# Kernel optimization log

Measured on AMD Instinct MI355X. Metric: run time of the kernel, lower is better.

The kernel has to match this reference:

```python
import jax, jax.numpy as jnp
import numpy as np

B = 16; L_IN = 512; D_MODEL = 512; N_HEAD = 8; D_K = 128; D_V = 128
D_FF = 2048; N_LAYER = 4; WINDOW = (4, 4, 4); INNER = 5; COV = 4; NUM_SEQ = 128
N_LVL = len(WINDOW) + 1


def _build_mask_sizes():
    # Pyraformer get_mask: intra-scale band + inter-scale parent/child links.
    all_size = [L_IN]
    for w in WINDOW:
        all_size.append(all_size[-1] // w)
    L = sum(all_size)
    vis = np.zeros((L, L), dtype=bool)
    iw = INNER // 2
    starts = [0]
    for s in all_size:
        starts.append(starts[-1] + s)
    for li, sz in enumerate(all_size):
        s = starts[li]
        for i in range(s, s + sz):
            vis[i, max(i - iw, s):min(i + iw + 1, s + sz)] = True
    for li in range(1, len(all_size)):
        s = starts[li]
        for i in range(s, s + all_size[li]):
            l = (s - all_size[li - 1]) + (i - s) * WINDOW[li - 1]
            if i == s + all_size[li] - 1:
                r = s
            else:
                r = (s - all_size[li - 1]) + (i - s + 1) * WINDOW[li - 1]
            vis[i, l:r] = True
            vis[l:r, i] = True
    return ~vis, all_size  # True = blocked


def _build_indexes(all_size):
    # Pyraformer refer_points: for each fine position, its ancestor at each scale.
    idx = np.zeros((L_IN, len(all_size)), dtype=np.int64)
    for i in range(L_IN):
        idx[i, 0] = i
        former = i
        for j in range(1, len(all_size)):
            start = sum(all_size[:j])
            inner = former - (start - all_size[j - 1])
            former = start + min(inner // WINDOW[j - 1], all_size[j] - 1)
            idx[i, j] = former
    return idx


def _layer_norm(x, g, b, eps=1e-5):
    m = x.mean(-1, keepdims=True)
    v = x.var(-1, keepdims=True)
    return (x - m) / jnp.sqrt(v + eps) * g + b


def _conv1d(x, w, stride):  # x: [B,C,L], w: [O,I,K]
    return jax.lax.conv_general_dilated(x, w, (stride,), 'VALID',
                                        dimension_numbers=('NCH', 'OIH', 'NCH'))


def _forward(x, cov_w, cov_b, data_conv_w, down_w, down_b, conv_w, conv_b, bn_g, bn_b,
             up_w, up_b, bln_g, bln_b, wq, wk, wv, fc_w, ln1_g, ln1_b,
             ffn_w1, ffn_b1, ffn_w2, ffn_b2, ln2_g, ln2_b, attn_mask, gather_idx):
    Bsz = x.shape[0]
    # SingleStepEmbedding
    covs = jnp.concatenate([x[:, :, 1:1 + COV], (x[:, :, -1] / NUM_SEQ - 0.5)[..., None]], -1)
    cov_emb = covs @ cov_w + cov_b
    data = x[:, :, 0][:, None, :]                      # [B,1,L]
    data = jnp.concatenate([data[:, :, -1:], data, data[:, :, :1]], -1)  # circular pad k=3
    data_emb = _conv1d(data, data_conv_w, 1).transpose(0, 2, 1)          # [B,L,D]
    i = jnp.arange(D_MODEL)
    vec = jnp.power(10000.0, 2.0 * (i // 2) / D_MODEL)
    ang = jnp.arange(L_IN)[:, None] / vec
    pos_emb = jnp.where(i % 2 == 0, jnp.sin(ang), jnp.cos(ang))
    seq = cov_emb + data_emb + pos_emb[None]
    # Bottleneck_Construct (down -> strided convs -> up -> concat -> LN)
    tmp = (seq @ down_w + down_b).transpose(0, 2, 1)   # [B,d_k,L]
    outs = []
    for s in range(len(WINDOW)):
        tmp = _conv1d(tmp, conv_w[s], WINDOW[s]) + conv_b[s][None, :, None]
        mu = tmp.mean((0, 2), keepdims=True)
        var = tmp.var((0, 2), keepdims=True)
        tmp = (tmp - mu) / jnp.sqrt(var + 1e-5) * bn_g[s][None, :, None] + bn_b[s][None, :, None]
        tmp = jax.nn.elu(tmp)
        outs.append(tmp)
    pyr = jnp.concatenate(outs, axis=2).transpose(0, 2, 1) @ up_w + up_b
    enc = _layer_norm(jnp.concatenate([seq, pyr], axis=1), bln_g, bln_b)  # [B,Ltot,D]
    Lt = enc.shape[1]
    scale = np.float32(1.0 / np.sqrt(D_K))
    for l in range(N_LAYER):
        q = (enc @ wq[l]).reshape(Bsz, Lt, N_HEAD, D_K).transpose(0, 2, 1, 3)
        k = (enc @ wk[l]).reshape(Bsz, Lt, N_HEAD, D_K).transpose(0, 2, 1, 3)
        v = (enc @ wv[l]).reshape(Bsz, Lt, N_HEAD, D_V).transpose(0, 2, 1, 3)
        scores = jnp.einsum('bhqd,bhkd->bhqk', q, k) * scale
        scores = jnp.where(attn_mask[None, None], -1e9, scores)
        attn = jax.nn.softmax(scores, -1)
        o = jnp.einsum('bhqk,bhkd->bhqd', attn, v).transpose(0, 2, 1, 3).reshape(Bsz, Lt, N_HEAD * D_V)
        enc = _layer_norm(o @ fc_w[l] + enc, ln1_g[l], ln1_b[l])  # post-norm
        h = jax.nn.gelu(enc @ ffn_w1[l] + ffn_b1[l], approximate=False) @ ffn_w2[l] + ffn_b2[l]
        enc = _layer_norm(enc + h, ln2_g[l], ln2_b[l])
    # refer_points gather: [B, L_IN, N_LVL*D]
    out = enc[:, gather_idx.reshape(-1), :].reshape(Bsz, L_IN, N_LVL * D_MODEL)
    return out


def setup_inputs() -> dict:
    key = jax.random.key(0)
    ks = iter(jax.random.split(key, 64))

    def nrm(shape, scale=0.02):
        return (jax.random.normal(next(ks), shape) * scale).astype(jnp.float32)

    covs = jax.random.normal(next(ks), (B, L_IN, COV + 1), jnp.float32)
    ids = jax.random.randint(next(ks), (B, L_IN), 0, NUM_SEQ).astype(jnp.float32)
    x = jnp.concatenate([covs, ids[..., None]], -1)  # col0=data, 1..COV=covs, last=series id
    mask_np, all_size = _build_mask_sizes()
    idx = _build_indexes(all_size)
    nw = len(WINDOW)
    return dict(
        x=x,
        cov_w=nrm((COV + 1, D_MODEL)), cov_b=jnp.zeros((D_MODEL,), jnp.float32),
        data_conv_w=nrm((D_MODEL, 1, 3)),
        down_w=nrm((D_MODEL, D_K)), down_b=jnp.zeros((D_K,), jnp.float32),
        conv_w=nrm((nw, D_K, D_K, WINDOW[0])), conv_b=jnp.zeros((nw, D_K), jnp.float32),
        bn_g=jnp.ones((nw, D_K), jnp.float32), bn_b=jnp.zeros((nw, D_K), jnp.float32),
        up_w=nrm((D_K, D_MODEL)), up_b=jnp.zeros((D_MODEL,), jnp.float32),
        bln_g=jnp.ones((D_MODEL,), jnp.float32), bln_b=jnp.zeros((D_MODEL,), jnp.float32),
        wq=nrm((N_LAYER, D_MODEL, N_HEAD * D_K)), wk=nrm((N_LAYER, D_MODEL, N_HEAD * D_K)),
        wv=nrm((N_LAYER, D_MODEL, N_HEAD * D_V)), fc_w=nrm((N_LAYER, N_HEAD * D_V, D_MODEL)),
        ln1_g=jnp.ones((N_LAYER, D_MODEL), jnp.float32), ln1_b=jnp.zeros((N_LAYER, D_MODEL), jnp.float32),
        ffn_w1=nrm((N_LAYER, D_MODEL, D_FF)), ffn_b1=jnp.zeros((N_LAYER, D_FF), jnp.float32),
        ffn_w2=nrm((N_LAYER, D_FF, D_MODEL)), ffn_b2=jnp.zeros((N_LAYER, D_MODEL), jnp.float32),
        ln2_g=jnp.ones((N_LAYER, D_MODEL), jnp.float32), ln2_b=jnp.zeros((N_LAYER, D_MODEL), jnp.float32),
        attn_mask=jnp.asarray(mask_np),
        gather_idx=jnp.asarray(idx),
    )


def reference(x, cov_w, cov_b, data_conv_w, down_w, down_b, conv_w, conv_b, bn_g, bn_b,
              up_w, up_b, bln_g, bln_b, wq, wk, wv, fc_w, ln1_g, ln1_b,
              ffn_w1, ffn_b1, ffn_w2, ffn_b2, ln2_g, ln2_b, attn_mask, gather_idx):
    return _forward(x, cov_w, cov_b, data_conv_w, down_w, down_b, conv_w, conv_b, bn_g, bn_b,
                    up_w, up_b, bln_g, bln_b, wq, wk, wv, fc_w, ln1_g, ln1_b,
                    ffn_w1, ffn_b1, ffn_w2, ffn_b2, ln2_g, ln2_b, attn_mask, gather_idx)
```

## Files before the change

kernel.cpp:

```cpp
#include <hip/hip_runtime.h>
#include <math.h>

typedef unsigned short u16;
typedef unsigned int u32;
typedef __attribute__((ext_vector_type(8))) short s16x8;
typedef __attribute__((ext_vector_type(4))) float f32x4;
typedef __attribute__((ext_vector_type(4))) u32 u32x4;
typedef __attribute__((ext_vector_type(2))) u32 u32x2;

#define LT 680

static __device__ __forceinline__ float bf2f(u16 u) {
  u32 v = ((u32)u) << 16;
  return __builtin_bit_cast(float, v);
}
static __device__ __forceinline__ u16 f2bf(float f) {
  u32 u = __builtin_bit_cast(u32, f);
  u32 r = (u + 0x7FFFu + ((u >> 16) & 1u)) >> 16;
  return (u16)r;
}
static __device__ __forceinline__ float lo16(u32 u) {
  return __builtin_bit_cast(float, u << 16);
}
static __device__ __forceinline__ float hi16(u32 u) {
  return __builtin_bit_cast(float, u & 0xFFFF0000u);
}

static __device__ __forceinline__ void gload16(const u16* g, u16* l) {
  __builtin_amdgcn_global_load_lds(
      (const __attribute__((address_space(1))) u32*)g,
      (__attribute__((address_space(3))) u32*)l, 16, 0, 0);
}

__global__ void detect_k(const u32* __restrict__ blng, int* __restrict__ flag) {
  if (threadIdx.x == 0 && blockIdx.x == 0)
    *flag = (blng[0] == 0x3F803F80u) ? 1 : 0;
}

struct CvtArgs {
  const void* src[20];
  float* dst[20];
  int pre[21];
};

__global__ __launch_bounds__(256) void cvtall_k(CvtArgs a, const int* __restrict__ flag) {
  int i = blockIdx.x * 256 + threadIdx.x;
  if (i >= a.pre[20]) return;
  int s = 0;
#pragma unroll
  for (int k = 1; k <= 20; ++k)
    if (i >= a.pre[k]) s = k;
  int j = i - a.pre[s];
  bool isb = (*flag != 0);
  a.dst[s][j] = isb ? bf2f(((const u16*)a.src[s])[j]) : ((const float*)a.src[s])[j];
}

__global__ __launch_bounds__(256) void tc2_k(const void* __restrict__ S,
                                             u16* __restrict__ D, int K, int N,
                                             size_t sstride, size_t dstride,
                                             const int* __restrict__ flag) {
  __shared__ u16 t[32][33];
  size_t soff = (size_t)blockIdx.z * sstride;
  D += (size_t)blockIdx.z * dstride;
  int nb = blockIdx.x * 32, kb = blockIdx.y * 32;
  int lx = threadIdx.x & 31, ly = threadIdx.x >> 5;
  bool isb = (*flag != 0);
#pragma unroll
  for (int i = 0; i < 4; ++i) {
    size_t idx = soff + (size_t)(kb + ly + 8 * i) * N + nb + lx;
    t[ly + 8 * i][lx] = isb ? ((const u16*)S)[idx] : f2bf(((const float*)S)[idx]);
  }
  __syncthreads();
#pragma unroll
  for (int i = 0; i < 4; ++i)
    D[(size_t)(nb + ly + 8 * i) * K + kb + lx] = t[lx][ly + 8 * i];
}

static __device__ __forceinline__ void reduce2_256(float& a, float& b, float* sm) {
#pragma unroll
  for (int o = 32; o; o >>= 1) { a += __shfl_xor(a, o); b += __shfl_xor(b, o); }
  int w = threadIdx.x >> 6, ln = threadIdx.x & 63;
  if (ln == 0) { sm[w] = a; sm[4 + w] = b; }
  __syncthreads();
  a = sm[0] + sm[1] + sm[2] + sm[3];
  b = sm[4] + sm[5] + sm[6] + sm[7];
  __syncthreads();
}

__global__ __launch_bounds__(256) void emb_k(
    const float* __restrict__ x, const float* __restrict__ covw,
    const float* __restrict__ covb, const float* __restrict__ dw,
    float* __restrict__ seq) {
  int r = blockIdx.x;
  int b = r >> 9, l = r & 511;
  int base = r * 6;
  float c0 = x[base + 1], c1 = x[base + 2];
  float c2 = x[base + 3], c3 = x[base + 4];
  float c4 = x[base + 5] * 0.0078125f - 0.5f;
  int lm = (l + 511) & 511, lp = (l + 1) & 511;
  float dm = x[((b << 9) + lm) * 6];
  float d0 = x[base];
  float dp = x[((b << 9) + lp) * 6];
  for (int d = threadIdx.x; d < 512; d += 256) {
    float cov = c0 * covw[d] + c1 * covw[512 + d] +
                c2 * covw[1024 + d] + c3 * covw[1536 + d] +
                c4 * covw[2048 + d] + covb[d];
    float cv = dm * dw[d * 3] + d0 * dw[d * 3 + 1] + dp * dw[d * 3 + 2];
    float ex = (float)(2 * (d >> 1)) * (1.0f / 512.0f);
    float vec = powf(10000.0f, ex);
    float ang = (float)l / vec;
    float pos = (d & 1) ? cosf(ang) : sinf(ang);
    seq[((size_t)r << 9) + d] = cov + cv + pos;
  }
}

__global__ void tconv_k(const float* __restrict__ w, float* __restrict__ wt) {
  int e = blockIdx.x * 256 + threadIdx.x;
  if (e >= 3 * 512 * 128) return;
  int o = e & 127, ik = (e >> 7) & 511, s = e >> 16;
  wt[e] = w[s * 65536 + o * 512 + ik];
}

__global__ __launch_bounds__(256) void gemm_k(
    const float* __restrict__ A, const float* __restrict__ Bw,
    const float* __restrict__ bias, float* __restrict__ C,
    int M, int N, int K, int act) {
  __shared__ float As[16][64];
  __shared__ float Bs[16][64];
  int tid = threadIdx.x;
  int m0 = blockIdx.y * 64, n0 = blockIdx.x * 64;
  int tx = tid & 15, ty = tid >> 4;
  int la_r = tid >> 2, la_c = (tid & 3) << 2;
  int lb_r = tid >> 4, lb_c = (tid & 15) << 2;
  float acc[4][4] = {};
  for (int k0 = 0; k0 < K; k0 += 16) {
    float4 av = *reinterpret_cast<const float4*>(A + (size_t)(m0 + la_r) * K + k0 + la_c);
    As[la_c + 0][la_r] = av.x;
    As[la_c + 1][la_r] = av.y;
    As[la_c + 2][la_r] = av.z;
    As[la_c + 3][la_r] = av.w;
    float4 bv = *reinterpret_cast<const float4*>(Bw + (size_t)(k0 + lb_r) * N + n0 + lb_c);
    Bs[lb_r][lb_c + 0] = bv.x;
    Bs[lb_r][lb_c + 1] = bv.y;
    Bs[lb_r][lb_c + 2] = bv.z;
    Bs[lb_r][lb_c + 3] = bv.w;
    __syncthreads();
#pragma unroll
    for (int kk = 0; kk < 16; ++kk) {
      float4 a4 = *reinterpret_cast<const float4*>(&As[kk][ty << 2]);
      float4 b4 = *reinterpret_cast<const float4*>(&Bs[kk][tx << 2]);
      float ar[4] = {a4.x, a4.y, a4.z, a4.w};
      float br[4] = {b4.x, b4.y, b4.z, b4.w};
#pragma unroll
      for (int i = 0; i < 4; ++i)
#pragma unroll
        for (int j = 0; j < 4; ++j) acc[i][j] = fmaf(ar[i], br[j], acc[i][j]);
    }
    __syncthreads();
  }
  float bj[4] = {0.f, 0.f, 0.f, 0.f};
  if (bias) {
#pragma unroll
    for (int j = 0; j < 4; ++j) bj[j] = bias[n0 + (tx << 2) + j];
  }
#pragma unroll
  for (int i = 0; i < 4; ++i) {
    float4 o;
    float* op = reinterpret_cast<float*>(&o);
#pragma unroll
    for (int j = 0; j < 4; ++j) op[j] = acc[i][j] + bj[j];
    *reinterpret_cast<float4*>(C + (size_t)(m0 + (ty << 2) + i) * N + n0 + (tx << 2)) = o;
  }
}

static __device__ __forceinline__ f32x4 mfma16(s16x8 a, s16x8 b, f32x4 c) {
  return __builtin_amdgcn_mfma_f32_16x16x32_bf16(a, b, c, 0, 0, 0);
}

__global__ __launch_bounds__(256) void mgemm_k(
    const u16* __restrict__ A, const u16* __restrict__ BT,
    const float* __restrict__ bias, void* __restrict__ C,
    int M, int N, int K, int flags) {
  __shared__ char smem[32768];
  float* st = (float*)smem;
  int tid = threadIdx.x;

  int nN = N >> 7;
  int nwg = gridDim.x;
  int bid = blockIdx.x;
  int qq = nwg >> 3, rr = nwg & 7;
  int xcd = bid & 7, lin = bid >> 3;
  int s_ = (xcd < rr ? xcd * (qq + 1) : rr * (qq + 1) + (xcd - rr) * qq) + lin;
  int m0 = (s_ / nN) << 7, n0 = (s_ % nN) << 7;

  int l = tid & 63, wid = tid >> 6;
  int wr = wid >> 1, wc = wid & 1;
  f32x4 acc[4][4];
#pragma unroll
  for (int i = 0; i < 4; ++i)
#pragma unroll
    for (int j = 0; j < 4; ++j)
#pragma unroll
      for (int r = 0; r < 4; ++r) acc[i][j][r] = 0.f;

  int L8 = l >> 3;
  int p0_ = (l & 7) ^ L8;
  int rloc = 2 * L8 + (p0_ >> 2);
  int cel = (p0_ & 3) << 3;
  const u16* Ag0 = A + (size_t)m0 * K;
  const u16* Bg0 = BT + (size_t)n0 * K;

  auto STAGE = [&](int c, int kt) {
    u16* Ad = (u16*)smem + c * 8192;
    u16* Bd = Ad + 4096;
#pragma unroll
    for (int i = 0; i < 2; ++i) {
      int rg = wid * 32 + i * 16 + rloc;
      gload16(Ag0 + (size_t)rg * K + kt + cel, &Ad[(wid * 16 + i * 8) * 64]);
      gload16(Bg0 + (size_t)rg * K + kt + cel, &Bd[(wid * 16 + i * 8) * 64]);
    }
  };

  int sfrag = (((l & 1) << 2) + (l >> 4)) ^ (((l & 15) >> 1));
  int lhalf = (l & 15) >> 1;

  int nt = K >> 5;
  STAGE(0, 0);
  for (int t = 0; t < nt; ++t) {
    int cur = t & 1;
    if (t + 1 < nt) {
      STAGE(cur ^ 1, (t + 1) << 5);
      asm volatile("s_waitcnt vmcnt(4)" ::: "memory");
    } else {
      asm volatile("s_waitcnt vmcnt(0)" ::: "memory");
    }
    __builtin_amdgcn_s_barrier();
    const u16* Asb = (const u16*)smem + cur * 8192;
    const u16* Bsb = Asb + 4096;
    s16x8 af[4];
#pragma unroll
    for (int fr = 0; fr < 4; ++fr)
      af[fr] = *reinterpret_cast<const s16x8*>(
          &Asb[(wr * 32 + fr * 8 + lhalf) * 64 + sfrag * 8]);
#pragma unroll
    for (int fc = 0; fc < 4; ++fc) {
      s16x8 bf = *reinterpret_cast<const s16x8*>(
          &Bsb[(wc * 32 + fc * 8 + lhalf) * 64 + sfrag * 8]);
#pragma unroll
      for (int fr = 0; fr < 4; ++fr)
        acc[fr][fc] = mfma16(af[fr], bf, acc[fr][fc]);
    }
    asm volatile("s_waitcnt lgkmcnt(0)" ::: "memory");
    __builtin_amdgcn_s_barrier();
  }

  int cl = l & 15, rg2 = l >> 4;
  float bj[4];
#pragma unroll
  for (int fc = 0; fc < 4; ++fc)
    bj[fc] = bias ? bias[n0 + wc * 64 + fc * 16 + cl] : 0.f;
  int sr2 = tid >> 3;
  int scg = (tid & 7) << 4;
  int growb = m0 + ((sr2 >> 4) << 6) + (sr2 & 15);
#pragma unroll
  for (int fr = 0; fr < 4; ++fr) {
#pragma unroll
    for (int fc = 0; fc < 4; ++fc) {
      int col = wc * 64 + fc * 16 + cl;
#pragma unroll
      for (int r = 0; r < 4; ++r) {
        float v = acc[fr][fc][r] + bj[fc];
        if (flags & 2) {
          float zz = 1.5957691f * fmaf(0.044715f * v, v * v, v);
          v = v / (1.0f + __expf(-zz));
        }
        st[(wr * 16 + rg2 * 4 + r) * 132 + col] = v;
      }
    }
    __syncthreads();
    int gr = growb + fr * 16;
    if (flags & 1) {
      u32x4 o0, o1;
      u16* p0 = (u16*)&o0; u16* p1 = (u16*)&o1;
#pragma unroll
      for (int i = 0; i < 8; ++i) p0[i] = f2bf(st[sr2 * 132 + scg + i]);
#pragma unroll
      for (int i = 0; i < 8; ++i) p1[i] = f2bf(st[sr2 * 132 + scg + 8 + i]);
      u16* dst = (u16*)C + (size_t)gr * N + n0 + scg;
      __builtin_nontemporal_store(o0, reinterpret_cast<u32x4*>(dst));
      __builtin_nontemporal_store(o1, reinterpret_cast<u32x4*>(dst + 8));
    } else {
      float* dst = (float*)C + (size_t)gr * N + n0 + scg;
#pragma unroll
      for (int i = 0; i < 4; ++i)
        __builtin_nontemporal_store(
            *reinterpret_cast<const f32x4*>(&st[sr2 * 132 + scg + 4 * i]),
            reinterpret_cast<f32x4*>(dst + 4 * i));
    }
    __syncthreads();
  }
}

__global__ __launch_bounds__(256) void mgemm64_k(
    const u16* __restrict__ A, const u16* __restrict__ BT,
    const float* __restrict__ bias, float* __restrict__ C,
    int M, int N, int K) {
  __shared__ char smem[49152];
  float* st = (float*)smem;
  int tid = threadIdx.x;

  int nN = N >> 6;
  int nwg = gridDim.x;
  int bid = blockIdx.x;
  int qq = nwg >> 3, rr = nwg & 7;
  int xcd = bid & 7, lin = bid >> 3;
  int s_ = (xcd < rr ? xcd * (qq + 1) : rr * (qq + 1) + (xcd - rr) * qq) + lin;
  int m0 = (s_ / nN) << 7, n0 = (s_ % nN) << 6;

  int l = tid & 63, wid = tid >> 6;
  f32x4 acc[2][4];
#pragma unroll
  for (int i = 0; i < 2; ++i)
#pragma unroll
    for (int j = 0; j < 4; ++j)
#pragma unroll
      for (int r = 0; r < 4; ++r) acc[i][j][r] = 0.f;

  int row8 = l >> 3, cp = l & 7;
  int cg = (cp ^ (row8 & 7)) << 3;
  const u16* Ag0 = A + (size_t)m0 * K;
  const u16* Bg0 = BT + (size_t)n0 * K;

  auto STAGE = [&](int c, int kt) {
    u16* Ad = (u16*)smem + c * 12288;
    u16* Bd = Ad + 8192;
    int rbA = wid * 32;
#pragma unroll
    for (int i = 0; i < 4; ++i) {
      int r = rbA + i * 8 + row8;
      gload16(Ag0 + (size_t)r * K + kt + cg, &Ad[(rbA + i * 8) * 64]);
    }
    int rbB = wid * 16;
#pragma unroll
    for (int i = 0; i < 2; ++i) {
      int r = rbB + i * 8 + row8;
      gload16(Bg0 + (size_t)r * K + kt + cg, &Bd[(rbB + i * 8) * 64]);
    }
  };

  int nt = K >> 6;
  STAGE(0, 0);
  for (int t = 0; t < nt; ++t) {
    int cur = t & 1;
    if (t + 1 < nt) {
      STAGE(cur ^ 1, (t + 1) << 6);
      asm volatile("s_waitcnt vmcnt(6)" ::: "memory");
    } else {
      asm volatile("s_waitcnt vmcnt(0)" ::: "memory");
    }
    __builtin_amdgcn_s_barrier();
    const u16* Asb = (const u16*)smem + cur * 12288;
    const u16* Bsb = Asb + 8192;
#pragma unroll
    for (int kk = 0; kk < 2; ++kk) {
      int kc = ((kk * 4 + (l >> 4)) ^ (l & 7)) * 8;
      s16x8 af[2];
#pragma unroll
      for (int fr = 0; fr < 2; ++fr)
        af[fr] = *reinterpret_cast<const s16x8*>(
            &Asb[(wid * 32 + fr * 16 + (l & 15)) * 64 + kc]);
#pragma unroll
      for (int fc = 0; fc < 4; ++fc) {
        s16x8 bf = *reinterpret_cast<const s16x8*>(
            &Bsb[(fc * 16 + (l & 15)) * 64 + kc]);
#pragma unroll
        for (int fr = 0; fr < 2; ++fr)
          acc[fr][fc] = mfma16(af[fr], bf, acc[fr][fc]);
      }
    }
    asm volatile("s_waitcnt lgkmcnt(0)" ::: "memory");
    __builtin_amdgcn_s_barrier();
  }

  int cl = l & 15, rg = l >> 4;
  float bj[4];
#pragma unroll
  for (int fc = 0; fc < 4; ++fc)
    bj[fc] = bias ? bias[n0 + fc * 16 + cl] : 0.f;
  int lr = tid >> 2;
  int lc = (tid & 3) << 4;
  int gr = m0 + ((lr >> 4) << 5) + (lr & 15);
#pragma unroll
  for (int fr = 0; fr < 2; ++fr) {
#pragma unroll
    for (int fc = 0; fc < 4; ++fc)
#pragma unroll
      for (int r = 0; r < 4; ++r)
        st[(wid * 16 + rg * 4 + r) * 68 + fc * 16 + cl] = acc[fr][fc][r] + bj[fc];
    __syncthreads();
    float* dst = C + (size_t)(gr + fr * 16) * N + n0 + lc;
#pragma unroll
    for (int i = 0; i < 4; ++i)
      __builtin_nontemporal_store(
          *reinterpret_cast<const f32x4*>(&st[lr * 68 + lc + 4 * i]),
          reinterpret_cast<f32x4*>(dst + 4 * i));
    __syncthreads();
  }
}

__global__ void im2col_k(const float* __restrict__ Y, float* __restrict__ X,
                         int Ti, int To) {
  int e = blockIdx.x * 256 + threadIdx.x;
  int ik = e & 511;
  int bt = e >> 9;
  int b = bt / To, t = bt - b * To;
  int i = ik >> 2, k = ik & 3;
  X[e] = Y[((size_t)(b * Ti + (t << 2) + k) << 7) + i];
}

__global__ __launch_bounds__(256) void bnelu_k(float* __restrict__ Y,
                                               const float* __restrict__ g,
                                               const float* __restrict__ be, int Ms) {
  __shared__ float sm[8];
  int ch = blockIdx.x;
  float s = 0.f, s2 = 0.f;
  for (int i = threadIdx.x; i < Ms; i += 256) {
    float v = Y[((size_t)i << 7) + ch];
    s += v; s2 += v * v;
  }
  reduce2_256(s, s2, sm);
  float mu = s / (float)Ms;
  float var = s2 / (float)Ms - mu * mu;
  float inv = rsqrtf(var + 1e-5f);
  float ga = g[ch], bb = be[ch];
  for (int i = threadIdx.x; i < Ms; i += 256) {
    float v = (Y[((size_t)i << 7) + ch] - mu) * inv * ga + bb;
    Y[((size_t)i << 7) + ch] = (v > 0.f) ? v : (expf(v) - 1.0f);
  }
}

__global__ void scat_k(const float* __restrict__ Y, float* __restrict__ cat,
                       int Ts, int off) {
  int e = blockIdx.x * 256 + threadIdx.x;
  int i = e & 127;
  int bt = e >> 7;
  int b = bt / Ts, t = bt - b * Ts;
  cat[((size_t)(b * 168 + off + t) << 7) + i] = Y[e];
}

__global__ __launch_bounds__(256) void catln_k(
    const float* __restrict__ seq, const float* __restrict__ pyr,
    const float* __restrict__ g, const float* __restrict__ be,
    float* __restrict__ out, u16* __restrict__ outb) {
  __shared__ float sm[8];
  int row = blockIdx.x;
  int b = row / LT, j = row - b * LT;
  const float* src = (j < 512) ? (seq + ((size_t)(b * 512 + j) << 9))
                               : (pyr + ((size_t)(b * 168 + j - 512) << 9));
  int t = threadIdx.x;
  float x0 = src[t], x1 = src[t + 256];
  float s = x0 + x1, s2 = x0 * x0 + x1 * x1;
  reduce2_256(s, s2, sm);
  float mu = s * 0.001953125f;
  float var = s2 * 0.001953125f - mu * mu;
  float inv = rsqrtf(var + 1e-5f);
  size_t ob = (size_t)row << 9;
  float v0 = (x0 - mu) * inv * g[t] + be[t];
  float v1 = (x1 - mu) * inv * g[t + 256] + be[t + 256];
  out[ob + t] = v0; out[ob + t + 256] = v1;
  outb[ob + t] = f2bf(v0); outb[ob + t + 256] = f2bf(v1);
}

__global__ __launch_bounds__(256) void lnres_k(
    const float* __restrict__ A, const float* __restrict__ R,
    const float* __restrict__ g, const float* __restrict__ be,
    float* __restrict__ O, u16* __restrict__ Ob) {
  __shared__ float sm[8];
  int row = blockIdx.x;
  size_t base = (size_t)row << 9;
  int t = threadIdx.x;
  float x0 = A[base + t] + R[base + t];
  float x1 = A[base + t + 256] + R[base + t + 256];
  float s = x0 + x1, s2 = x0 * x0 + x1 * x1;
  reduce2_256(s, s2, sm);
  float mu = s * 0.001953125f;
  float var = s2 * 0.001953125f - mu * mu;
  float inv = rsqrtf(var + 1e-5f);
  float v0 = (x0 - mu) * inv * g[t] + be[t];
  float v1 = (x1 - mu) * inv * g[t + 256] + be[t + 256];
  O[base + t] = v0; O[base + t + 256] = v1;
  Ob[base + t] = f2bf(v0); Ob[base + t + 256] = f2bf(v1);
}

__global__ __launch_bounds__(256) void attn_k(const u16* __restrict__ QKV,
                                              u16* __restrict__ O) {
  int cpx = gridDim.x >> 3;
  int bq = (blockIdx.x & 7) * cpx + (blockIdx.x >> 3);
  int b = bq / LT, q = bq - b * LT;
  int lane = threadIdx.x & 63, wv = threadIdx.x >> 6;
  int half = lane >> 5, t4 = (lane & 31) << 2;
  int h = (wv << 1) + half;
  int lvl = (q < 512) ? 0 : (q < 640) ? 1 : (q < 672) ? 2 : 3;
  int Sl = (lvl == 0) ? 0 : (lvl == 1) ? 512 : (lvl == 2) ? 640 : 672;
  int SZl = (lvl == 0) ? 512 : (lvl == 1) ? 128 : (lvl == 2) ? 32 : 8;
  int p = q - Sl;
  int Sc = (lvl == 1) ? 0 : (lvl == 2) ? 512 : 640;
  int Sp = (lvl == 0) ? 512 : (lvl == 1) ? 640 : 672;
  int tg[10];
  bool vd[10];
#pragma unroll
  for (int jj = 0; jj < 10; ++jj) {
    int tgt; bool valid;
    if (jj < 5) { int pp = p - 2 + jj; valid = (pp >= 0 && pp < SZl); tgt = Sl + pp; }
    else if (jj < 9) { valid = (lvl > 0); tgt = Sc + p * 4 + (jj - 5); }
    else { valid = (lvl < 3); tgt = Sp + (p >> 2); }
    if (!valid) tgt = q;
    tg[jj] = tgt; vd[jj] = valid;
  }
  size_t hoff = h * 128 + t4;
  u32x2 qv = *reinterpret_cast<const u32x2*>(QKV + (size_t)bq * 3072 + hoff);
  float q0 = lo16(qv.x), q1 = hi16(qv.x), q2 = lo16(qv.y), q3 = hi16(qv.y);
  size_t base3 = (size_t)b * LT;
  float sc[10];
  float mx = -1e30f;
#pragma unroll
  for (int jj = 0; jj < 10; ++jj) {
    u32x2 kv = *reinterpret_cast<const u32x2*>(
        QKV + (base3 + tg[jj]) * 3072 + 1024 + hoff);
    float pr = q0 * lo16(kv.x) + q1 * hi16(kv.x) + q2 * lo16(kv.y) + q3 * hi16(kv.y);
#pragma unroll
    for (int o = 16; o; o >>= 1) pr += __shfl_xor(pr, o);
    float sv = vd[jj] ? pr * 0.08838834764831845f : -1e30f;
    sc[jj] = sv;
    mx = fmaxf(mx, sv);
  }
  float den = 0.f;
#pragma unroll
  for (int jj = 0; jj < 10; ++jj) { sc[jj] = expf(sc[jj] - mx); den += sc[jj]; }
  float invd = 1.0f / den;
  float o0 = 0.f, o1 = 0.f, o2 = 0.f, o3 = 0.f;
#pragma unroll
  for (int jj = 0; jj < 10; ++jj) {
    u32x2 vv = *reinterpret_cast<const u32x2*>(
        QKV + (base3 + tg[jj]) * 3072 + 2048 + hoff);
    float w = sc[jj] * invd;
    o0 = fmaf(w, lo16(vv.x), o0);
    o1 = fmaf(w, hi16(vv.x), o1);
    o2 = fmaf(w, lo16(vv.y), o2);
    o3 = fmaf(w, hi16(vv.y), o3);
  }
  u32x2 ov;
  ov.x = (u32)f2bf(o0) | ((u32)f2bf(o1) << 16);
  ov.y = (u32)f2bf(o2) | ((u32)f2bf(o3) << 16);
  *reinterpret_cast<u32x2*>(O + (size_t)bq * 1024 + hoff) = ov;
}

__global__ void gather_k(const float* __restrict__ enc, void* __restrict__ out,
                         const int* __restrict__ flag) {
  int e = blockIdx.x * 256 + threadIdx.x;
  int d = e & 511;
  int lvl = (e >> 9) & 3;
  int i = (e >> 11) & 511;
  int b = e >> 20;
  int g = (lvl == 0) ? i
        : (lvl == 1) ? (512 + (i >> 2))
        : (lvl == 2) ? (640 + (i >> 4))
                     : (672 + (i >> 6));
  float v = enc[(((size_t)b * LT + g) << 9) + d];
  if (*flag) ((u16*)out)[e] = f2bf(v);
  else       ((float*)out)[e] = v;
}

extern "C" void kernel_launch(void* const* d_in, const int* in_sizes, int n_in,
                              void* d_out, int out_size, void* d_ws, size_t ws_size,
                              hipStream_t stream) {
  float* ws = (float*)d_ws;
  size_t off = 0;
  auto alloc = [&](size_t n) { float* p = ws + off; off += (n + 63) & ~(size_t)63; return p; };

  int* flag = (int*)alloc(64);

  static const int cvt_n[26] = {
      49152, 2560, 512, 1536, 65536, 128, 196608, 384, 384, 384,
      65536, 512, 512, 512, 2097152, 2097152, 2097152, 2097152, 2048, 2048,
      4194304, 8192, 4194304, 2048, 2048, 2048};
  float* cf[26];
  for (int i = 0; i < 26; ++i) cf[i] = alloc(cvt_n[i]);

  float* cwt     = alloc(196608);
  float* enc     = alloc((size_t)10880 * 512);
  float* tmp     = alloc((size_t)10880 * 512);
  u16*   encb    = (u16*)alloc((size_t)10880 * 512 / 2);
  u16*   qkv     = (u16*)alloc((size_t)10880 * 3072 / 2);
  u16*   attnout = (u16*)alloc((size_t)10880 * 1024 / 2);
  u16*   qkvw    = (u16*)alloc((size_t)4 * 3072 * 512 / 2);
  u16*   fcT     = (u16*)alloc((size_t)4 * 512 * 1024 / 2);
  u16*   w1T     = (u16*)alloc((size_t)4 * 2048 * 512 / 2);
  u16*   w2T     = (u16*)alloc((size_t)4 * 512 * 2048 / 2);
  u16*   H1      = qkv;

  float* seq   = (float*)qkv;
  float* pyr   = seq + 4194304;
  float* tdown = pyr + 1376256;
  float* xcol  = tdown + 1048576;
  float* ya    = xcol + 1048576;
  float* yb    = ya + 262144;
  float* yc    = yb + 65536;
  float* cat   = yc + 16384;

  detect_k<<<1, 64, 0, stream>>>((const u32*)d_in[12], flag);
  {
    static const int segs[20] = {0,1,2,3,4,5,6,7,8,9,10,11,12,13,18,19,21,23,24,25};
    CvtArgs a;
    int acc_ = 0;
    for (int k = 0; k < 20; ++k) {
      int i = segs[k];
      a.src[k] = d_in[i];
      a.dst[k] = cf[i];
      a.pre[k] = acc_;
      acc_ += cvt_n[i];
    }
    a.pre[20] = acc_;
    cvtall_k<<<(acc_ + 255) / 256, 256, 0, stream>>>(a, flag);
  }

  const float *x = cf[0], *covw = cf[1], *covb = cf[2], *dconvw = cf[3],
              *downw = cf[4], *downb = cf[5], *convw = cf[6], *convb = cf[7],
              *bng = cf[8], *bnb = cf[9], *upw = cf[10], *upb = cf[11],
              *blng = cf[12], *blnb = cf[13], *ln1g = cf[18], *ln1b = cf[19],
              *b1 = cf[21], *b2 = cf[23], *ln2g = cf[24], *ln2b = cf[25];

  tc2_k<<<dim3(32, 16, 4), 256, 0, stream>>>(d_in[14], qkvw,           512, 1024, 524288, 1572864, flag);
  tc2_k<<<dim3(32, 16, 4), 256, 0, stream>>>(d_in[15], qkvw + 524288,  512, 1024, 524288, 1572864, flag);
  tc2_k<<<dim3(32, 16, 4), 256, 0, stream>>>(d_in[16], qkvw + 1048576, 512, 1024, 524288, 1572864, flag);
  tc2_k<<<dim3(16, 32, 4), 256, 0, stream>>>(d_in[17], fcT,  1024, 512, 524288, 524288, flag);
  tc2_k<<<dim3(64, 16, 4), 256, 0, stream>>>(d_in[20], w1T,  512, 2048, 1048576, 1048576, flag);
  tc2_k<<<dim3(16, 64, 4), 256, 0, stream>>>(d_in[22], w2T,  2048, 512, 1048576, 1048576, flag);

  emb_k<<<8192, 256, 0, stream>>>(x, covw, covb, dconvw, seq);
  tconv_k<<<(3 * 512 * 128 + 255) / 256, 256, 0, stream>>>(convw, cwt);

  gemm_k<<<dim3(2, 128), 256, 0, stream>>>(seq, downw, downb, tdown, 8192, 128, 512, 0);
  im2col_k<<<(16 * 128 * 512) / 256, 256, 0, stream>>>(tdown, xcol, 512, 128);
  gemm_k<<<dim3(2, 32), 256, 0, stream>>>(xcol, cwt, convb, ya, 2048, 128, 512, 0);
  bnelu_k<<<128, 256, 0, stream>>>(ya, bng, bnb, 2048);
  scat_k<<<(2048 * 128) / 256, 256, 0, stream>>>(ya, cat, 128, 0);
  im2col_k<<<(16 * 32 * 512) / 256, 256, 0, stream>>>(ya, xcol, 128, 32);
  gemm_k<<<dim3(2, 8), 256, 0, stream>>>(xcol, cwt + 65536, convb + 128, yb, 512, 128, 512, 0);
  bnelu_k<<<128, 256, 0, stream>>>(yb, bng + 128, bnb + 128, 512);
  scat_k<<<(512 * 128) / 256, 256, 0, stream>>>(yb, cat, 32, 128);
  im2col_k<<<(16 * 8 * 512) / 256, 256, 0, stream>>>(yb, xcol, 32, 8);
  gemm_k<<<dim3(2, 2), 256, 0, stream>>>(xcol, cwt + 131072, convb + 256, yc, 128, 128, 512, 0);
  bnelu_k<<<128, 256, 0, stream>>>(yc, bng + 256, bnb + 256, 128);
  scat_k<<<(128 * 128) / 256, 256, 0, stream>>>(yc, cat, 8, 160);
  gemm_k<<<dim3(8, 42), 256, 0, stream>>>(cat, upw, upb, pyr, 2688, 512, 128, 0);
  catln_k<<<10880, 256, 0, stream>>>(seq, pyr, blng, blnb, enc, encb);

  for (int l = 0; l < 4; ++l) {
    const u16* qw  = qkvw + (size_t)l * 3072 * 512;
    const u16* fw  = fcT + (size_t)l * 524288;
    const u16* w1w = w1T + (size_t)l * 1048576;
    const u16* w2w = w2T + (size_t)l * 1048576;
    mgemm_k<<<85 * 24, 256, 0, stream>>>(encb, qw, nullptr, qkv, 10880, 3072, 512, 1);
    attn_k<<<16 * LT, 256, 0, stream>>>(qkv, attnout);
    mgemm64_k<<<85 * 8, 256, 0, stream>>>(attnout, fw, nullptr, tmp, 10880, 512, 1024);
    lnres_k<<<10880, 256, 0, stream>>>(tmp, enc, ln1g + l * 512, ln1b + l * 512, enc, encb);
    mgemm_k<<<85 * 16, 256, 0, stream>>>(encb, w1w, b1 + l * 2048, H1, 10880, 2048, 512, 3);
    mgemm64_k<<<85 * 8, 256, 0, stream>>>(H1, w2w, b2 + l * 512, tmp, 10880, 512, 2048);
    lnres_k<<<10880, 256, 0, stream>>>(tmp, enc, ln2g + l * 512, ln2b + l * 512, enc, encb);
  }

  gather_k<<<(16 * 512 * 2048) / 256, 256, 0, stream>>>(enc, d_out, flag);
}
```

Baseline: 1.301 ms.

## Halve mgemm64 K-tile to 32 with repacked swizzled LDS layout

Reduces the K step of the 128x64 bf16 GEMM kernel from 64 to 32. LDS use drops from 48KB to 24KB, allowing more resident workgroups per CU, and two 32-wide rows are packed per 64-element LDS row with a new XOR swizzle for fragment reads. The epilogue store pattern is changed so each thread writes interleaved 16-byte chunks, which gives more coalesced row writes. In exchange there are twice as many loop iterations and barriers per K, with less work per prefetch to hide latency.

```diff
diff --git a/kernel.cpp b/kernel.cpp
--- a/kernel.cpp
+++ b/kernel.cpp
@@ -305,7 +305,7 @@
     const u16* __restrict__ A, const u16* __restrict__ BT,
     const float* __restrict__ bias, float* __restrict__ C,
     int M, int N, int K) {
-  __shared__ char smem[49152];
+  __shared__ char smem[24576];
   float* st = (float*)smem;
   int tid = threadIdx.x;
 
@@ -326,57 +326,55 @@
 #pragma unroll
       for (int r = 0; r < 4; ++r) acc[i][j][r] = 0.f;
 
-  int row8 = l >> 3, cp = l & 7;
-  int cg = (cp ^ (row8 & 7)) << 3;
+  int L8 = l >> 3;
+  int p0_ = (l & 7) ^ L8;
+  int rloc = 2 * L8 + (p0_ >> 2);
+  int cel = (p0_ & 3) << 3;
   const u16* Ag0 = A + (size_t)m0 * K;
   const u16* Bg0 = BT + (size_t)n0 * K;
 
   auto STAGE = [&](int c, int kt) {
-    u16* Ad = (u16*)smem + c * 12288;
-    u16* Bd = Ad + 8192;
-    int rbA = wid * 32;
-#pragma unroll
-    for (int i = 0; i < 4; ++i) {
-      int r = rbA + i * 8 + row8;
-      gload16(Ag0 + (size_t)r * K + kt + cg, &Ad[(rbA + i * 8) * 64]);
-    }
-    int rbB = wid * 16;
+    u16* Ad = (u16*)smem + c * 6144;
+    u16* Bd = Ad + 4096;
 #pragma unroll
     for (int i = 0; i < 2; ++i) {
-      int r = rbB + i * 8 + row8;
-      gload16(Bg0 + (size_t)r * K + kt + cg, &Bd[(rbB + i * 8) * 64]);
+      int rg = wid * 32 + i * 16 + rloc;
+      gload16(Ag0 + (size_t)rg * K + kt + cel, &Ad[(wid * 16 + i * 8) * 64]);
+    }
+    {
+      int rg = wid * 16 + rloc;
+      gload16(Bg0 + (size_t)rg * K + kt + cel, &Bd[(wid * 8) * 64]);
     }
   };
 
-  int nt = K >> 6;
+  int sfrag = (((l & 1) << 2) + (l >> 4)) ^ (((l & 15) >> 1));
+  int lhalf = (l & 15) >> 1;
+
+  int nt = K >> 5;
   STAGE(0, 0);
   for (int t = 0; t < nt; ++t) {
     int cur = t & 1;
     if (t + 1 < nt) {
-      STAGE(cur ^ 1, (t + 1) << 6);
-      asm volatile("s_waitcnt vmcnt(6)" ::: "memory");
+      STAGE(cur ^ 1, (t + 1) << 5);
+      asm volatile("s_waitcnt vmcnt(3)" ::: "memory");
     } else {
       asm volatile("s_waitcnt vmcnt(0)" ::: "memory");
     }
     __builtin_amdgcn_s_barrier();
-    const u16* Asb = (const u16*)smem + cur * 12288;
-    const u16* Bsb = Asb + 8192;
-#pragma unroll
-    for (int kk = 0; kk < 2; ++kk) {
-      int kc = ((kk * 4 + (l >> 4)) ^ (l & 7)) * 8;
-      s16x8 af[2];
+    const u16* Asb = (const u16*)smem + cur * 6144;
+    const u16* Bsb = Asb + 4096;
+    s16x8 af[2];
+#pragma unroll
+    for (int fr = 0; fr < 2; ++fr)
+      af[fr] = *reinterpret_cast<const s16x8*>(
+          &Asb[(wid * 16 + fr * 8 + lhalf) * 64 + sfrag * 8]);
+#pragma unroll
+    for (int fc = 0; fc < 4; ++fc) {
+      s16x8 bf = *reinterpret_cast<const s16x8*>(
+          &Bsb[(fc * 8 + lhalf) * 64 + sfrag * 8]);
 #pragma unroll
       for (int fr = 0; fr < 2; ++fr)
-        af[fr] = *reinterpret_cast<const s16x8*>(
-            &Asb[(wid * 32 + fr * 16 + (l & 15)) * 64 + kc]);
-#pragma unroll
-      for (int fc = 0; fc < 4; ++fc) {
-        s16x8 bf = *reinterpret_cast<const s16x8*>(
-            &Bsb[(fc * 16 + (l & 15)) * 64 + kc]);
-#pragma unroll
-        for (int fr = 0; fr < 2; ++fr)
-          acc[fr][fc] = mfma16(af[fr], bf, acc[fr][fc]);
-      }
+        acc[fr][fc] = mfma16(af[fr], bf, acc[fr][fc]);
     }
     asm volatile("s_waitcnt lgkmcnt(0)" ::: "memory");
     __builtin_amdgcn_s_barrier();
@@ -388,7 +386,7 @@
   for (int fc = 0; fc < 4; ++fc)
     bj[fc] = bias ? bias[n0 + fc * 16 + cl] : 0.f;
   int lr = tid >> 2;
-  int lc = (tid & 3) << 4;
+  int lcq = (tid & 3) << 2;
   int gr = m0 + ((lr >> 4) << 5) + (lr & 15);
 #pragma unroll
   for (int fr = 0; fr < 2; ++fr) {
@@ -398,12 +396,12 @@
       for (int r = 0; r < 4; ++r)
         st[(wid * 16 + rg * 4 + r) * 68 + fc * 16 + cl] = acc[fr][fc][r] + bj[fc];
     __syncthreads();
-    float* dst = C + (size_t)(gr + fr * 16) * N + n0 + lc;
+    float* dst = C + (size_t)(gr + fr * 16) * N + n0;
 #pragma unroll
     for (int i = 0; i < 4; ++i)
       __builtin_nontemporal_store(
-          *reinterpret_cast<const f32x4*>(&st[lr * 68 + lc + 4 * i]),
-          reinterpret_cast<f32x4*>(dst + 4 * i));
+          *reinterpret_cast<const f32x4*>(&st[lr * 68 + lcq + 16 * i]),
+          reinterpret_cast<f32x4*>(dst + lcq + 16 * i));
     __syncthreads();
   }
 }
```

Measured after the change: 1.229 ms. -5.5%, faster.
